# Performance work log

Measured on AMD Instinct MI355X. Metric: run time of the kernel, lower is better.

Reference implementation:

```python
import jax, jax.numpy as jnp
import numpy as np

BANDWIDTH = 1.0  # init kwarg: bandwidth; sphere mode -> var_s = gamma = bandwidth
LOG2PI = float(np.log(2.0 * np.pi))


def setup_inputs() -> dict:
    key = jax.random.key(0)
    k1, k2, k3, k4 = jax.random.split(key, 4)
    x = jax.random.normal(k1, (4096, 256), dtype=jnp.float32)
    y = jax.random.normal(k2, (4096, 128), dtype=jnp.float32)
    x_s = jax.random.normal(k3, (8192, 256), dtype=jnp.float32)
    y_s = jax.random.normal(k4, (8192, 128), dtype=jnp.float32)
    return {"x": x, "y": y, "x_s": x_s, "y_s": y_s}


def _sq_dists(a, b):
    # ||a_i - b_j||^2 via GEMM expansion: (batch, num_s)
    a2 = jnp.sum(a * a, axis=-1)[:, None]
    b2 = jnp.sum(b * b, axis=-1)[None, :]
    return a2 + b2 - 2.0 * jnp.einsum("bd,sd->bs", a, b)


def reference(x, y, x_s, y_s):
    x_dim = x.shape[-1]
    y_dim = y.shape[-1]
    var_s = BANDWIDTH
    gamma = BANDWIDTH
    logA_x = x_dim * (LOG2PI + jnp.log(jnp.float32(var_s)))
    logA_y = y_dim * (LOG2PI + jnp.log(jnp.float32(gamma)))

    sdx = _sq_dists(x, x_s) / var_s  # (batch, num_s)
    sdy = _sq_dists(y, y_s) / gamma  # (batch, num_s)

    E_log_pxy = jax.nn.logsumexp(-0.5 * (logA_x + logA_y + sdx + sdy), axis=-1)
    E_log_px = jax.nn.logsumexp(-0.5 * (logA_x + sdx), axis=-1)
    E_log_py = jax.nn.logsumexp(-0.5 * (logA_y + sdy), axis=-1)
    return jnp.mean(E_log_pxy - E_log_px - E_log_py)
```

## Files before the change

### kernel.cpp

```cpp
#include <hip/hip_runtime.h>
#include <hip/hip_bf16.h>
#include <stdint.h>

#define B_N 4096
#define S_N 8192
#define KX  256
#define KY  128
#define BM 128
#define BN 128

typedef __bf16 bf16x8 __attribute__((ext_vector_type(8)));
typedef float  f32x4  __attribute__((ext_vector_type(4)));

#define OFF_XH   ((size_t)0)
#define OFF_YH   ((size_t)2097152)
#define OFF_SXH  ((size_t)3145728)
#define OFF_SYH  ((size_t)7340032)
#define OFF_NX   ((size_t)9437184)
#define OFF_NY   (OFF_NX + 16384)
#define OFF_NSX  (OFF_NY + 16384)
#define OFF_NSY  (OFF_NSX + 32768)
#define OFF_PART (OFF_NSY + 32768)
#define OFF_BSUM (OFF_PART + (size_t)3*64*4096*2*4)

__device__ __forceinline__ void gl2lds16(const void* g, void* l) {
  typedef const __attribute__((address_space(1))) unsigned int* gp_t;
  typedef __attribute__((address_space(3))) unsigned int* lp_t;
  __builtin_amdgcn_global_load_lds((gp_t)g, (lp_t)l, 16, 0, 0);
}

__device__ __forceinline__ unsigned short f2bf(float f) {
  unsigned u = __builtin_bit_cast(unsigned, f);
  return (unsigned short)((u + 0x7fffu + ((u >> 16) & 1u)) >> 16);
}

__global__ __launch_bounds__(256) void conv_all(const float* __restrict__ x,
                                                const float* __restrict__ y,
                                                const float* __restrict__ xs,
                                                const float* __restrict__ ys,
                                                char* __restrict__ ws) {
  int b    = blockIdx.x;
  int wave = threadIdx.x >> 6;
  int lane = threadIdx.x & 63;
  const float* src; unsigned short* hi; float* nrm;
  int K, row;
  if (b < 1024) {
    src = x;  hi = (unsigned short*)(ws + OFF_XH);
    nrm = (float*)(ws + OFF_NX); K = 256; row = b * 4 + wave;
  } else if (b < 2048) {
    src = y;  hi = (unsigned short*)(ws + OFF_YH);
    nrm = (float*)(ws + OFF_NY); K = 128; row = (b - 1024) * 4 + wave;
  } else if (b < 4096) {
    src = xs; hi = (unsigned short*)(ws + OFF_SXH);
    nrm = (float*)(ws + OFF_NSX); K = 256; row = (b - 2048) * 4 + wave;
  } else {
    src = ys; hi = (unsigned short*)(ws + OFF_SYH);
    nrm = (float*)(ws + OFF_NSY); K = 128; row = (b - 4096) * 4 + wave;
  }
  float acc = 0.f;
  if (K == 256) {
    float4 v = ((const float4*)(src + (size_t)row * 256))[lane];
    float vv[4] = {v.x, v.y, v.z, v.w};
    ushort4 h4;
    unsigned short* hp = (unsigned short*)&h4;
    #pragma unroll
    for (int k = 0; k < 4; ++k) {
      hp[k] = f2bf(vv[k]);
      acc = fmaf(vv[k], vv[k], acc);
    }
    ((ushort4*)(hi + (size_t)row * 256))[lane] = h4;
  } else {
    float2 v = ((const float2*)(src + (size_t)row * 128))[lane];
    float vv[2] = {v.x, v.y};
    ushort2 h2;
    unsigned short* hp = (unsigned short*)&h2;
    #pragma unroll
    for (int k = 0; k < 2; ++k) {
      hp[k] = f2bf(vv[k]);
      acc = fmaf(vv[k], vv[k], acc);
    }
    ((ushort2*)(hi + (size_t)row * 128))[lane] = h2;
  }
  #pragma unroll
  for (int o = 32; o > 0; o >>= 1) acc += __shfl_down(acc, o);
  if (lane == 0) nrm[row] = acc;
}

__global__ __launch_bounds__(512, 4) void mie_main(const char* __restrict__ ws,
                                                   float* __restrict__ part) {
  __shared__ __align__(16) char smem[65536];

  const int tid  = threadIdx.x;
  const int lane = tid & 63;
  const int wave = tid >> 6;
  const int c    = lane & 15;
  const int q    = lane >> 4;
  const int wm   = wave >> 1;
  const int wn   = wave & 1;

  const int b     = blockIdx.x;
  const int xcd   = b & 7;
  const int w     = b >> 3;
  const int bm_t  = w & 31;
  const int sn_t  = xcd * 8 + (w >> 5);
  const int bm0   = bm_t * BM;
  const int sn0   = sn_t * BN;

  const char* xh  = ws + OFF_XH;
  const char* yh  = ws + OFF_YH;
  const char* sxh = ws + OFF_SXH;
  const char* syh = ws + OFF_SYH;
  const float* nx  = (const float*)(ws + OFF_NX);
  const float* ny  = (const float*)(ws + OFF_NY);
  const float* nsx = (const float*)(ws + OFF_NSX);
  const float* nsy = (const float*)(ws + OFF_NSY);

  const int r  = tid >> 2;
  const int sg = (tid & 3) ^ ((r >> 1) & 3);
  const char* aXp = xh  + (size_t)(bm0 + r) * 512 + sg * 16;
  const char* aYp = yh  + (size_t)(bm0 + r) * 256 + sg * 16;
  const char* bXp = sxh + (size_t)(sn0 + r) * 512 + sg * 16;
  const char* bYp = syh + (size_t)(sn0 + r) * 256 + sg * 16;
  char* sdst = smem + wave * 1024;

  const int slot  = (q ^ ((c >> 1) & 3)) * 16;
  const int aoff0 = (wm * 32 +  0 + c) * 64 + slot;
  const int aoff1 = (wm * 32 + 16 + c) * 64 + slot;
  const int boff0 = (wn * 64 +  0 + c) * 64 + slot;
  const int boff1 = (wn * 64 + 16 + c) * 64 + slot;
  const int boff2 = (wn * 64 + 32 + c) * 64 + slot;
  const int boff3 = (wn * 64 + 48 + c) * 64 + slot;

  f32x4 accx[2][4], accy[2][4];
  #pragma unroll
  for (int i = 0; i < 2; ++i)
    #pragma unroll
    for (int j = 0; j < 4; ++j) {
      accx[i][j] = (f32x4){0.f,0.f,0.f,0.f};
      accy[i][j] = (f32x4){0.f,0.f,0.f,0.f};
    }

#define STAGE(kc) do {                                                      \
    const char* _sa; const char* _sb;                                       \
    if ((kc) < 8) { _sa = aXp + (kc) * 64;       _sb = bXp + (kc) * 64; }   \
    else          { _sa = aYp + ((kc) - 8) * 64; _sb = bYp + ((kc) - 8) * 64; } \
    char* _d = sdst + ((kc) & 3) * 16384;                                   \
    gl2lds16(_sa, _d);                                                      \
    gl2lds16(_sb, _d + 8192);                                               \
  } while (0)

#define MFMA8(ACC, A0, A1, B0, B1, B2, B3) do {                                   \
    ACC[0][0] = __builtin_amdgcn_mfma_f32_16x16x32_bf16(A0, B0, ACC[0][0], 0,0,0); \
    ACC[0][1] = __builtin_amdgcn_mfma_f32_16x16x32_bf16(A0, B1, ACC[0][1], 0,0,0); \
    ACC[0][2] = __builtin_amdgcn_mfma_f32_16x16x32_bf16(A0, B2, ACC[0][2], 0,0,0); \
    ACC[0][3] = __builtin_amdgcn_mfma_f32_16x16x32_bf16(A0, B3, ACC[0][3], 0,0,0); \
    ACC[1][0] = __builtin_amdgcn_mfma_f32_16x16x32_bf16(A1, B0, ACC[1][0], 0,0,0); \
    ACC[1][1] = __builtin_amdgcn_mfma_f32_16x16x32_bf16(A1, B1, ACC[1][1], 0,0,0); \
    ACC[1][2] = __builtin_amdgcn_mfma_f32_16x16x32_bf16(A1, B2, ACC[1][2], 0,0,0); \
    ACC[1][3] = __builtin_amdgcn_mfma_f32_16x16x32_bf16(A1, B3, ACC[1][3], 0,0,0); \
  } while (0)

#define KSTEP(kc, vm, ACC) do {                                             \
    if ((kc) + 3 < 12) STAGE((kc) + 3);                                     \
    asm volatile("s_waitcnt vmcnt(" #vm ")" ::: "memory");                  \
    __builtin_amdgcn_s_barrier();                                           \
    asm volatile("" ::: "memory");                                          \
    const char* _base = smem + ((kc) & 3) * 16384;                          \
    bf16x8 _A0 = *(const bf16x8*)(_base + aoff0);                           \
    bf16x8 _A1 = *(const bf16x8*)(_base + aoff1);                           \
    bf16x8 _B0 = *(const bf16x8*)(_base + 8192 + boff0);                    \
    bf16x8 _B1 = *(const bf16x8*)(_base + 8192 + boff1);                    \
    bf16x8 _B2 = *(const bf16x8*)(_base + 8192 + boff2);                    \
    bf16x8 _B3 = *(const bf16x8*)(_base + 8192 + boff3);                    \
    __builtin_amdgcn_s_setprio(1);                                          \
    MFMA8(ACC, _A0, _A1, _B0, _B1, _B2, _B3);                               \
    __builtin_amdgcn_s_setprio(0);                                          \
    asm volatile("" ::: "memory");                                          \
    __builtin_amdgcn_s_barrier();                                           \
    asm volatile("" ::: "memory");                                          \
  } while (0)

  STAGE(0); STAGE(1); STAGE(2);

  KSTEP(0, 6, accx);  KSTEP(1, 6, accx);  KSTEP(2, 6, accx);  KSTEP(3, 6, accx);
  KSTEP(4, 6, accx);  KSTEP(5, 6, accx);  KSTEP(6, 6, accx);  KSTEP(7, 6, accx);
  KSTEP(8, 6, accy);  KSTEP(9, 4, accy);  KSTEP(10, 2, accy); KSTEP(11, 0, accy);

#undef KSTEP
#undef MFMA8
#undef STAGE

  float hxv[2][4], hyv[2][4];
  #pragma unroll
  for (int i = 0; i < 2; ++i)
    #pragma unroll
    for (int rr4 = 0; rr4 < 4; ++rr4) {
      int rr = bm0 + wm * 32 + i * 16 + q * 4 + rr4;
      hxv[i][rr4] = -0.5f * nx[rr];
      hyv[i][rr4] = -0.5f * ny[rr];
    }
  float hsxv[4], hsyv[4];
  #pragma unroll
  for (int j = 0; j < 4; ++j) {
    int cc = sn0 + wn * 64 + j * 16 + c;
    hsxv[j] = -0.5f * nsx[cc];
    hsyv[j] = -0.5f * nsy[cc];
  }

  float2* xch = (float2*)smem;
  #pragma unroll
  for (int i = 0; i < 2; ++i) {
    #pragma unroll
    for (int rr4 = 0; rr4 < 4; ++rr4) {
      float vx[4], vy[4];
      #pragma unroll
      for (int j = 0; j < 4; ++j) {
        vx[j] = accx[i][j][rr4] + hxv[i][rr4] + hsxv[j];
        vy[j] = accy[i][j][rr4] + hyv[i][rr4] + hsyv[j];
      }
      int rl = wm * 32 + i * 16 + q * 4 + rr4;
      #pragma unroll
      for (int st = 0; st < 3; ++st) {
        float v0 = (st == 0) ? vx[0] + vy[0] : (st == 1 ? vx[0] : vy[0]);
        float v1 = (st == 0) ? vx[1] + vy[1] : (st == 1 ? vx[1] : vy[1]);
        float v2 = (st == 0) ? vx[2] + vy[2] : (st == 1 ? vx[2] : vy[2]);
        float v3 = (st == 0) ? vx[3] + vy[3] : (st == 1 ? vx[3] : vy[3]);
        float m = fmaxf(fmaxf(v0, v1), fmaxf(v2, v3));
        #pragma unroll
        for (int msk = 1; msk < 16; msk <<= 1) m = fmaxf(m, __shfl_xor(m, msk));
        float s = __expf(v0 - m) + __expf(v1 - m) + __expf(v2 - m) + __expf(v3 - m);
        #pragma unroll
        for (int msk = 1; msk < 16; msk <<= 1) s += __shfl_xor(s, msk);
        if (c == 0) xch[(st * 128 + rl) * 2 + wn] = (float2){m, s};
      }
    }
  }
  __syncthreads();

  if (tid < 384) {
    int st = tid >> 7;
    int rl = tid & 127;
    float2 a = xch[(st * 128 + rl) * 2 + 0];
    float2 bb = xch[(st * 128 + rl) * 2 + 1];
    float m = fmaxf(a.x, bb.x);
    float s = a.y * __expf(a.x - m) + bb.y * __expf(bb.x - m);
    size_t idx = ((size_t)st * 64 + sn_t) * B_N + (bm0 + rl);
    ((float2*)part)[idx] = (float2){m, s};
  }
}

__global__ __launch_bounds__(256) void fin1(const float* __restrict__ part,
                                            float* __restrict__ bsum) {
  __shared__ float2 lds[3][4][64];
  int tid  = threadIdx.x;
  int wave = tid >> 6;
  int lane = tid & 63;
  int row  = blockIdx.x * 64 + lane;
  #pragma unroll
  for (int j = 0; j < 3; ++j) {
    float m = -__builtin_inff(), s = 0.f;
    #pragma unroll
    for (int pp = 0; pp < 16; ++pp) {
      int p = wave * 16 + pp;
      float2 a = ((const float2*)part)[((size_t)j * 64 + p) * B_N + row];
      float nm = fmaxf(m, a.x);
      s = s * __expf(m - nm) + a.y * __expf(a.x - nm);
      m = nm;
    }
    lds[j][wave][lane] = (float2){m, s};
  }
  __syncthreads();
  if (wave == 0) {
    float v[3];
    #pragma unroll
    for (int j = 0; j < 3; ++j) {
      float m = -__builtin_inff(), s = 0.f;
      #pragma unroll
      for (int u = 0; u < 4; ++u) {
        float2 a = lds[j][u][lane];
        float nm = fmaxf(m, a.x);
        s = s * __expf(m - nm) + a.y * __expf(a.x - nm);
        m = nm;
      }
      v[j] = m + __logf(s);
    }
    float local = v[0] - v[1] - v[2];
    #pragma unroll
    for (int o = 32; o > 0; o >>= 1) local += __shfl_down(local, o);
    if (lane == 0) bsum[blockIdx.x] = local;
  }
}

__global__ void fin2(const float* __restrict__ bsum, float* __restrict__ out) {
  int t = threadIdx.x;
  float a = bsum[t];
  #pragma unroll
  for (int o = 32; o > 0; o >>= 1) a += __shfl_down(a, o);
  if (t == 0) out[0] = a * (1.0f / (float)B_N);
}

extern "C" void kernel_launch(void* const* d_in, const int* in_sizes, int n_in,
                              void* d_out, int out_size, void* d_ws, size_t ws_size,
                              hipStream_t stream) {
  (void)in_sizes; (void)n_in; (void)out_size; (void)ws_size;
  const float* x  = (const float*)d_in[0];
  const float* y  = (const float*)d_in[1];
  const float* xs = (const float*)d_in[2];
  const float* ys = (const float*)d_in[3];
  char* ws = (char*)d_ws;

  conv_all<<<6144, 256, 0, stream>>>(x, y, xs, ys, ws);
  mie_main<<<2048, 512, 0, stream>>>(ws, (float*)(ws + OFF_PART));
  fin1<<<B_N / 64, 256, 0, stream>>>((const float*)(ws + OFF_PART), (float*)(ws + OFF_BSUM));
  fin2<<<1, 64, 0, stream>>>((const float*)(ws + OFF_BSUM), (float*)d_out);
}
```

Baseline: 145.8 us.

## Use one barrier per K-step and defer shuffle reduction to LDS

The K loop now issues the next global-to-LDS stage after the current fragments are read from LDS. This lets it drop the trailing barrier, leaving one barrier per iteration, with vmcnt thresholds adjusted to match. The epilogue replaces the four-level shuffle max/sum reduction with a single xor-8 merge. It writes 16 partials per row to LDS, which are then merged serially by one thread per row. This trades cross-lane shuffles for more LDS traffic and more exponentials in the final merge.

```diff
diff --git a/kernel.cpp b/kernel.cpp
--- a/kernel.cpp
+++ b/kernel.cpp
@@ -160,8 +160,7 @@
     ACC[1][3] = __builtin_amdgcn_mfma_f32_16x16x32_bf16(A1, B3, ACC[1][3], 0,0,0); \
   } while (0)
 
-#define KSTEP(kc, vm, ACC) do {                                             \
-    if ((kc) + 3 < 12) STAGE((kc) + 3);                                     \
+#define ITER(kc, vm, ACC) do {                                              \
     asm volatile("s_waitcnt vmcnt(" #vm ")" ::: "memory");                  \
     __builtin_amdgcn_s_barrier();                                           \
     asm volatile("" ::: "memory");                                          \
@@ -172,21 +171,19 @@
     bf16x8 _B1 = *(const bf16x8*)(_base + 8192 + boff1);                    \
     bf16x8 _B2 = *(const bf16x8*)(_base + 8192 + boff2);                    \
     bf16x8 _B3 = *(const bf16x8*)(_base + 8192 + boff3);                    \
+    if ((kc) + 3 < 12) STAGE((kc) + 3);                                     \
     __builtin_amdgcn_s_setprio(1);                                          \
     MFMA8(ACC, _A0, _A1, _B0, _B1, _B2, _B3);                               \
     __builtin_amdgcn_s_setprio(0);                                          \
-    asm volatile("" ::: "memory");                                          \
-    __builtin_amdgcn_s_barrier();                                           \
-    asm volatile("" ::: "memory");                                          \
   } while (0)
 
   STAGE(0); STAGE(1); STAGE(2);
 
-  KSTEP(0, 6, accx);  KSTEP(1, 6, accx);  KSTEP(2, 6, accx);  KSTEP(3, 6, accx);
-  KSTEP(4, 6, accx);  KSTEP(5, 6, accx);  KSTEP(6, 6, accx);  KSTEP(7, 6, accx);
-  KSTEP(8, 6, accy);  KSTEP(9, 4, accy);  KSTEP(10, 2, accy); KSTEP(11, 0, accy);
-
-#undef KSTEP
+  ITER(0, 4, accx);  ITER(1, 4, accx);  ITER(2, 4, accx);  ITER(3, 4, accx);
+  ITER(4, 4, accx);  ITER(5, 4, accx);  ITER(6, 4, accx);  ITER(7, 4, accx);
+  ITER(8, 4, accy);  ITER(9, 4, accy);  ITER(10, 2, accy); ITER(11, 0, accy);
+
+#undef ITER
 #undef MFMA8
 #undef STAGE
 
@@ -207,7 +204,7 @@
     hsyv[j] = -0.5f * nsy[cc];
   }
 
-  float2* xch = (float2*)smem;
+  float2* xch2 = (float2*)smem;
   #pragma unroll
   for (int i = 0; i < 2; ++i) {
     #pragma unroll
@@ -226,12 +223,12 @@
         float v2 = (st == 0) ? vx[2] + vy[2] : (st == 1 ? vx[2] : vy[2]);
         float v3 = (st == 0) ? vx[3] + vy[3] : (st == 1 ? vx[3] : vy[3]);
         float m = fmaxf(fmaxf(v0, v1), fmaxf(v2, v3));
-        #pragma unroll
-        for (int msk = 1; msk < 16; msk <<= 1) m = fmaxf(m, __shfl_xor(m, msk));
         float s = __expf(v0 - m) + __expf(v1 - m) + __expf(v2 - m) + __expf(v3 - m);
-        #pragma unroll
-        for (int msk = 1; msk < 16; msk <<= 1) s += __shfl_xor(s, msk);
-        if (c == 0) xch[(st * 128 + rl) * 2 + wn] = (float2){m, s};
+        float mo = __shfl_xor(m, 8);
+        float so = __shfl_xor(s, 8);
+        float nm = fmaxf(m, mo);
+        float ns = s * __expf(m - nm) + so * __expf(mo - nm);
+        if (c < 8) xch2[(st * 128 + rl) * 16 + wn * 8 + c] = (float2){nm, ns};
       }
     }
   }
@@ -240,10 +237,17 @@
   if (tid < 384) {
     int st = tid >> 7;
     int rl = tid & 127;
-    float2 a = xch[(st * 128 + rl) * 2 + 0];
-    float2 bb = xch[(st * 128 + rl) * 2 + 1];
-    float m = fmaxf(a.x, bb.x);
-    float s = a.y * __expf(a.x - m) + bb.y * __expf(bb.x - m);
+    const float2* row = xch2 + (st * 128 + rl) * 16;
+    int p0 = rl & 15;
+    float2 a = row[p0];
+    float m = a.x, s = a.y;
+    #pragma unroll
+    for (int p = 1; p < 16; ++p) {
+      float2 e = row[(p0 + p) & 15];
+      float nm = fmaxf(m, e.x);
+      s = s * __expf(m - nm) + e.y * __expf(e.x - nm);
+      m = nm;
+    }
     size_t idx = ((size_t)st * 64 + sn_t) * B_N + (bm0 + rl);
     ((float2*)part)[idx] = (float2){m, s};
   }
```

Measured after the change: 130.5 us. 1.12x faster.
